# Optimization experiments

Hardware: AMD Instinct MI355X
Metric: run time of the kernel (lower is better)

Reference implementation:

```python
import jax, jax.numpy as jnp
import numpy as np

B, T, C, H = 8, 1024, 768, 12
HD = C // H  # 64

def setup_inputs() -> dict:
    key = jax.random.key(0)
    ks = jax.random.split(key, 5)
    s = 0.02
    return {
        "x": jax.random.normal(ks[0], (B, T, C), dtype=jnp.float32),
        "w_attn": jax.random.normal(ks[1], (C, 3 * C), dtype=jnp.float32) * s,
        "b_attn": jnp.zeros((3 * C,), dtype=jnp.float32),
        "w_proj": jax.random.normal(ks[2], (C, C), dtype=jnp.float32) * s,
        "b_proj": jnp.zeros((C,), dtype=jnp.float32),
    }

def reference(x, w_attn, b_attn, w_proj, b_proj):
    Bx, Tx, Cx = x.shape
    qkv = x @ w_attn + b_attn                      # [B,T,3C]
    q, k, v = jnp.split(qkv, 3, axis=-1)
    # [B,H,T,hd]
    q = q.reshape(Bx, Tx, H, HD).transpose(0, 2, 1, 3)
    k = k.reshape(Bx, Tx, H, HD).transpose(0, 2, 1, 3)
    v = v.reshape(Bx, Tx, H, HD).transpose(0, 2, 1, 3)
    scale = 1.0 / jnp.sqrt(jnp.asarray(HD, dtype=x.dtype))
    scores = jnp.einsum('bhqd,bhkd->bhqk', q, k) * scale  # [B,H,T,T]
    causal = jnp.tril(jnp.ones((Tx, Tx), dtype=bool))
    scores = jnp.where(causal, scores, jnp.asarray(-jnp.inf, dtype=x.dtype))
    weights = jax.nn.softmax(scores, axis=-1)
    y = jnp.einsum('bhqk,bhkd->bhqd', weights, v)  # [B,H,T,hd]
    y = y.transpose(0, 2, 1, 3).reshape(Bx, Tx, Cx)
    return y @ w_proj + b_proj
```

## Files before the change

kernel.cpp:

```cpp
#include <hip/hip_runtime.h>
#include <cstdint>
#include <cstddef>

#define B_  8
#define T_  1024
#define C_  768
#define H_  12
#define HD_ 64
#define K3_ 2304

typedef unsigned short u16;
typedef __attribute__((ext_vector_type(8))) short bf16x8;
typedef __attribute__((ext_vector_type(4))) float f32x4;

#define MFMA __builtin_amdgcn_mfma_f32_16x16x32_bf16

__device__ __forceinline__ u16 f2bf(float f) {
    unsigned u = __builtin_bit_cast(unsigned, f);
    u += 0x7fffu + ((u >> 16) & 1u);
    return (u16)(u >> 16);
}

__device__ __forceinline__ unsigned pk2bf(float a, float b) {
    unsigned ua = __builtin_bit_cast(unsigned, a) + 0x8000u;
    unsigned ub = __builtin_bit_cast(unsigned, b) + 0x8000u;
    return (ua >> 16) | (ub & 0xffff0000u);
}

#define GLL16(gp, lp) __builtin_amdgcn_global_load_lds( \
    (__attribute__((address_space(1))) unsigned int*)(gp), \
    (__attribute__((address_space(3))) unsigned int*)(lp), 16, 0, 0)

__global__ void cvt_f32_bf16(const float* __restrict__ in, u16* __restrict__ out, int n4) {
    int i = blockIdx.x * blockDim.x + threadIdx.x;
    if (i < n4) {
        float4 v = ((const float4*)in)[i];
        ushort4 o;
        o.x = f2bf(v.x); o.y = f2bf(v.y); o.z = f2bf(v.z); o.w = f2bf(v.w);
        ((ushort4*)out)[i] = o;
    }
}

__global__ void tcvt(const float* __restrict__ in, u16* __restrict__ out, int R, int Cc) {
    __shared__ float tile[32][33];
    int bc = blockIdx.x * 32, br = blockIdx.y * 32;
    int tx = threadIdx.x, ty = threadIdx.y;
    #pragma unroll
    for (int kk = 0; kk < 32; kk += 8)
        tile[ty + kk][tx] = in[(size_t)(br + ty + kk) * Cc + bc + tx];
    __syncthreads();
    #pragma unroll
    for (int kk = 0; kk < 32; kk += 8)
        out[(size_t)(bc + ty + kk) * R + br + tx] = f2bf(tile[tx][ty + kk]);
}

__launch_bounds__(256)
__global__ void gemm_qkv(const u16* __restrict__ A, const u16* __restrict__ Bt,
                         const float* __restrict__ bias,
                         u16* __restrict__ q, u16* __restrict__ k, u16* __restrict__ v) {
    const int K = C_;
    __shared__ __align__(16) u16 SM[16896];
    u16 (*As)[32] = (u16(*)[32])SM;
    u16 (*Bs)[32] = (u16(*)[32])(SM + 4096);
    u16 (*Cs)[132] = (u16(*)[132])SM;
    int tid = threadIdx.x;
    int m0 = blockIdx.y * 128, n0 = blockIdx.x * 128;
    int lane = tid & 63, wv = tid >> 6;
    int wm = (wv >> 1) * 64, wn = (wv & 1) * 64;
    int r16 = lane & 15, quad = lane >> 4;

    f32x4 acc[4][4] = {};
    int row = tid >> 2, colb = (tid & 3) * 8;
    const u16* Ag0 = A  + (size_t)(m0 + row) * K + colb;
    const u16* Ag1 = A  + (size_t)(m0 + 64 + row) * K + colb;
    const u16* Bg0 = Bt + (size_t)(n0 + row) * K + colb;
    const u16* Bg1 = Bt + (size_t)(n0 + 64 + row) * K + colb;
    u16* Al0 = &As[row][colb];
    u16* Al1 = &As[64 + row][colb];
    u16* Bl0 = &Bs[row][colb];
    u16* Bl1 = &Bs[64 + row][colb];

    for (int kt = 0; kt < K; kt += 32) {
        GLL16(Ag0 + kt, Al0);
        GLL16(Ag1 + kt, Al1);
        GLL16(Bg0 + kt, Bl0);
        GLL16(Bg1 + kt, Bl1);
        __syncthreads();
        bf16x8 af[4], bfr[4];
        #pragma unroll
        for (int i = 0; i < 4; i++) af[i]  = *(const bf16x8*)&As[wm + i * 16 + r16][quad * 8];
        #pragma unroll
        for (int j = 0; j < 4; j++) bfr[j] = *(const bf16x8*)&Bs[wn + j * 16 + r16][quad * 8];
        #pragma unroll
        for (int i = 0; i < 4; i++)
            #pragma unroll
            for (int j = 0; j < 4; j++)
                acc[i][j] = MFMA(af[i], bfr[j], acc[i][j], 0, 0, 0);
        __syncthreads();
    }

    int sec = n0 / C_;
    int cc0 = n0 - sec * C_;
    int b = m0 >> 10, t0 = m0 & 1023;

    if (sec == 2) {
        #pragma unroll
        for (int i = 0; i < 4; i++) {
            #pragma unroll
            for (int j = 0; j < 4; j++) {
                int cc = cc0 + wn + j * 16 + r16;
                float bv = bias[2 * C_ + cc];
                int h = cc >> 6, hd = cc & 63;
                int t = t0 + wm + i * 16 + quad * 4;
                ushort4 ov;
                ov.x = f2bf(acc[i][j][0] + bv); ov.y = f2bf(acc[i][j][1] + bv);
                ov.z = f2bf(acc[i][j][2] + bv); ov.w = f2bf(acc[i][j][3] + bv);
                *(ushort4*)(v + (((size_t)b * H_ + h) * HD_ + hd) * T_ + t) = ov;
            }
        }
    } else {
        float scale = (sec == 0) ? 0.125f : 1.0f;
        u16* dst = (sec == 0) ? q : k;
        #pragma unroll
        for (int i = 0; i < 4; i++)
            #pragma unroll
            for (int j = 0; j < 4; j++) {
                int col = wn + j * 16 + r16;
                float bv = bias[sec * C_ + cc0 + col];
                #pragma unroll
                for (int r = 0; r < 4; r++)
                    Cs[wm + i * 16 + quad * 4 + r][col] = f2bf((acc[i][j][r] + bv) * scale);
            }
        __syncthreads();
        int h0 = cc0 >> 6;
        int rsel = tid >> 4;
        int hs = (tid >> 3) & 1;
        int c8 = (tid & 7) * 8;
        #pragma unroll
        for (int p = 0; p < 8; p++) {
            int rl = p * 16 + rsel;
            uint4 val = *(const uint4*)&Cs[rl][hs * 64 + c8];
            *(uint4*)(dst + (((size_t)b * H_ + h0 + hs) * T_ + t0 + rl) * HD_ + c8) = val;
        }
    }
}

__launch_bounds__(256)
__global__ void gemm_proj(const u16* __restrict__ A, const u16* __restrict__ Bt,
                          const float* __restrict__ bias, float* __restrict__ out) {
    const int K = C_, N = C_;
    __shared__ __align__(16) u16 As[128][32];
    __shared__ __align__(16) u16 Bs[128][32];
    int tid = threadIdx.x;
    int m0 = blockIdx.y * 128, n0 = blockIdx.x * 128;
    int lane = tid & 63, wv = tid >> 6;
    int wm = (wv >> 1) * 64, wn = (wv & 1) * 64;
    int r16 = lane & 15, quad = lane >> 4;

    f32x4 acc[4][4] = {};
    int row = tid >> 2, colb = (tid & 3) * 8;
    const u16* Ag0 = A  + (size_t)(m0 + row) * K + colb;
    const u16* Ag1 = A  + (size_t)(m0 + 64 + row) * K + colb;
    const u16* Bg0 = Bt + (size_t)(n0 + row) * K + colb;
    const u16* Bg1 = Bt + (size_t)(n0 + 64 + row) * K + colb;
    u16* Al0 = &As[row][colb];
    u16* Al1 = &As[64 + row][colb];
    u16* Bl0 = &Bs[row][colb];
    u16* Bl1 = &Bs[64 + row][colb];

    for (int kt = 0; kt < K; kt += 32) {
        GLL16(Ag0 + kt, Al0);
        GLL16(Ag1 + kt, Al1);
        GLL16(Bg0 + kt, Bl0);
        GLL16(Bg1 + kt, Bl1);
        __syncthreads();
        bf16x8 af[4], bfr[4];
        #pragma unroll
        for (int i = 0; i < 4; i++) af[i]  = *(const bf16x8*)&As[wm + i * 16 + r16][quad * 8];
        #pragma unroll
        for (int j = 0; j < 4; j++) bfr[j] = *(const bf16x8*)&Bs[wn + j * 16 + r16][quad * 8];
        #pragma unroll
        for (int i = 0; i < 4; i++)
            #pragma unroll
            for (int j = 0; j < 4; j++)
                acc[i][j] = MFMA(af[i], bfr[j], acc[i][j], 0, 0, 0);
        __syncthreads();
    }

    #pragma unroll
    for (int i = 0; i < 4; i++) {
        #pragma unroll
        for (int j = 0; j < 4; j++) {
            int gn = n0 + wn + j * 16 + r16;
            float bv = bias[gn];
            #pragma unroll
            for (int r = 0; r < 4; r++) {
                int gm = m0 + wm + i * 16 + quad * 4 + r;
                out[(size_t)gm * N + gn] = acc[i][j][r] + bv;
            }
        }
    }
}

__launch_bounds__(256, 2)
__global__ void attn(const u16* __restrict__ q, const u16* __restrict__ k,
                     const u16* __restrict__ v, u16* __restrict__ y) {
    __shared__ __align__(16) u16 Kb[2][64][64];
    __shared__ __align__(16) u16 Vb[2][64][64];
    __shared__ __align__(16) u16 P[4][2][16][72];
    int tid = threadIdx.x, lane = tid & 63, w = tid >> 6;
    int r16 = lane & 15, quad = lane >> 4;
    int id = blockIdx.x;
    int bh = id % 96;
    int bi = id / 96;
    int b = bh / H_, h = bh - b * H_;
    int x = bi * 4 + w;
    int t_lo = x, t_hi = 63 - x;
    int qb_lo = t_lo * 16, qb_hi = t_hi * 16;
    const u16* qh = q + (size_t)bh * T_ * HD_;
    const u16* kh = k + (size_t)bh * T_ * HD_;
    const u16* vh = v + (size_t)bh * HD_ * T_;

    bf16x8 ql0 = *(const bf16x8*)(qh + (size_t)(qb_lo + r16) * HD_ + quad * 8);
    bf16x8 ql1 = *(const bf16x8*)(qh + (size_t)(qb_lo + r16) * HD_ + 32 + quad * 8);
    bf16x8 qh0 = *(const bf16x8*)(qh + (size_t)(qb_hi + r16) * HD_ + quad * 8);
    bf16x8 qh1 = *(const bf16x8*)(qh + (size_t)(qb_hi + r16) * HD_ + 32 + quad * 8);

    f32x4 oL[4] = {}, oH[4] = {};
    float lL = 0.f, lH = 0.f;
    int qyL = qb_lo + r16, qyH = qb_hi + r16;
    int ilo_last = bi;
    int n64 = __builtin_amdgcn_readfirstlane(16 - bi);

    int srow = lane >> 3;
    int scb  = (lane & 7) ^ srow;
    const u16* kst = kh + (size_t)(w * 16 + srow) * HD_ + scb * 8;
    const u16* vst = vh + (size_t)(w * 16 + srow) * T_ + scb * 8;
    int swz = (r16 & 7);

    {
        #pragma unroll
        for (int s2 = 0; s2 < 2; s2++) {
            GLL16(kst + (size_t)(s2 * 8) * HD_, &Kb[0][w * 16 + s2 * 8][0] + lane * 8);
            GLL16(vst + (size_t)(s2 * 8) * T_,  &Vb[0][w * 16 + s2 * 8][0] + lane * 8);
        }
    }
    __syncthreads();

    for (int it = 0; it < n64; ++it) {
        int kv0 = it * 64;
        int buf = it & 1;
        bool lo_on = (it <= ilo_last);
        if (it + 1 < n64) {
            int kvn = kv0 + 64;
            #pragma unroll
            for (int s2 = 0; s2 < 2; s2++) {
                GLL16(kst + (size_t)(kvn + s2 * 8) * HD_, &Kb[buf ^ 1][w * 16 + s2 * 8][0] + lane * 8);
                GLL16(vst + (size_t)(s2 * 8) * T_ + kvn,  &Vb[buf ^ 1][w * 16 + s2 * 8][0] + lane * 8);
            }
        }
        bf16x8 kf[4][2];
        #pragma unroll
        for (int n = 0; n < 4; n++)
            #pragma unroll
            for (int c = 0; c < 2; c++)
                kf[n][c] = *(const bf16x8*)&Kb[buf][n * 16 + r16][((c * 4 + quad) ^ swz) * 8];
        f32x4 sH[4] = {};
        #pragma unroll
        for (int n = 0; n < 4; n++) {
            sH[n] = MFMA(kf[n][0], qh0, sH[n], 0, 0, 0);
            sH[n] = MFMA(kf[n][1], qh1, sH[n], 0, 0, 0);
        }
        if (it == n64 - 1) {
            #pragma unroll
            for (int n = 0; n < 4; n++)
                #pragma unroll
                for (int r = 0; r < 4; r++)
                    if (kv0 + n * 16 + quad * 4 + r > qyH) sH[n][r] = -1e30f;
        }
        #pragma unroll
        for (int n = 0; n < 4; n++) {
            float p0 = __expf(sH[n][0]);
            float p1 = __expf(sH[n][1]);
            float p2 = __expf(sH[n][2]);
            float p3 = __expf(sH[n][3]);
            lH += (p0 + p1) + (p2 + p3);
            uint2 pd; pd.x = pk2bf(p0, p1); pd.y = pk2bf(p2, p3);
            *(uint2*)&P[w][1][r16][n * 16 + quad * 4] = pd;
        }
        if (lo_on) {
            f32x4 sL[4] = {};
            #pragma unroll
            for (int n = 0; n < 4; n++) {
                sL[n] = MFMA(kf[n][0], ql0, sL[n], 0, 0, 0);
                sL[n] = MFMA(kf[n][1], ql1, sL[n], 0, 0, 0);
            }
            if (it == ilo_last) {
                #pragma unroll
                for (int n = 0; n < 4; n++)
                    #pragma unroll
                    for (int r = 0; r < 4; r++)
                        if (kv0 + n * 16 + quad * 4 + r > qyL) sL[n][r] = -1e30f;
            }
            #pragma unroll
            for (int n = 0; n < 4; n++) {
                float p0 = __expf(sL[n][0]);
                float p1 = __expf(sL[n][1]);
                float p2 = __expf(sL[n][2]);
                float p3 = __expf(sL[n][3]);
                lL += (p0 + p1) + (p2 + p3);
                uint2 pd; pd.x = pk2bf(p0, p1); pd.y = pk2bf(p2, p3);
                *(uint2*)&P[w][0][r16][n * 16 + quad * 4] = pd;
            }
        }
        bf16x8 vf[4][2];
        #pragma unroll
        for (int j = 0; j < 4; j++)
            #pragma unroll
            for (int c = 0; c < 2; c++)
                vf[j][c] = *(const bf16x8*)&Vb[buf][j * 16 + r16][((c * 4 + quad) ^ swz) * 8];
        #pragma unroll
        for (int c = 0; c < 2; c++) {
            bf16x8 pfH = *(const bf16x8*)&P[w][1][r16][c * 32 + quad * 8];
            #pragma unroll
            for (int j = 0; j < 4; j++)
                oH[j] = MFMA(vf[j][c], pfH, oH[j], 0, 0, 0);
        }
        if (lo_on) {
            #pragma unroll
            for (int c = 0; c < 2; c++) {
                bf16x8 pfL = *(const bf16x8*)&P[w][0][r16][c * 32 + quad * 8];
                #pragma unroll
                for (int j = 0; j < 4; j++)
                    oL[j] = MFMA(vf[j][c], pfL, oL[j], 0, 0, 0);
            }
        }
        __syncthreads();
    }

    lH += __shfl_xor(lH, 16, 64);
    lH += __shfl_xor(lH, 32, 64);
    lL += __shfl_xor(lL, 16, 64);
    lL += __shfl_xor(lL, 32, 64);
    float invH = 1.f / lH, invL = 1.f / lL;
    int tqH = qb_hi + r16, tqL = qb_lo + r16;
    #pragma unroll
    for (int j = 0; j < 4; j++) {
        ushort4 ovH, ovL;
        ovH.x = f2bf(oH[j][0] * invH); ovH.y = f2bf(oH[j][1] * invH);
        ovH.z = f2bf(oH[j][2] * invH); ovH.w = f2bf(oH[j][3] * invH);
        ovL.x = f2bf(oL[j][0] * invL); ovL.y = f2bf(oL[j][1] * invL);
        ovL.z = f2bf(oL[j][2] * invL); ovL.w = f2bf(oL[j][3] * invL);
        *(ushort4*)(y + ((size_t)b * T_ + tqH) * C_ + h * 64 + j * 16 + quad * 4) = ovH;
        *(ushort4*)(y + ((size_t)b * T_ + tqL) * C_ + h * 64 + j * 16 + quad * 4) = ovL;
    }
}

extern "C" void kernel_launch(void* const* d_in, const int* in_sizes, int n_in,
                              void* d_out, int out_size, void* d_ws, size_t ws_size,
                              hipStream_t stream) {
    const float* x      = (const float*)d_in[0];
    const float* w_attn = (const float*)d_in[1];
    const float* b_attn = (const float*)d_in[2];
    const float* w_proj = (const float*)d_in[3];
    const float* b_proj = (const float*)d_in[4];
    float* out = (float*)d_out;

    char* ws = (char*)d_ws;
    size_t off = 0;
    auto alloc = [&](size_t bytes) {
        void* p = ws + off;
        off += (bytes + 255) & ~(size_t)255;
        return p;
    };
    const size_t M = (size_t)B_ * T_;
    u16* x_bf = (u16*)alloc(M * C_ * 2);
    u16* wat  = (u16*)alloc((size_t)K3_ * C_ * 2);
    u16* wpt  = (u16*)alloc((size_t)C_ * C_ * 2);
    u16* qb   = (u16*)alloc((size_t)B_ * H_ * T_ * HD_ * 2);
    u16* kb   = (u16*)alloc((size_t)B_ * H_ * T_ * HD_ * 2);
    u16* vb   = (u16*)alloc((size_t)B_ * H_ * T_ * HD_ * 2);
    u16* yb   = (u16*)alloc(M * C_ * 2);

    cvt_f32_bf16<<<(int)(M * C_ / 4 / 256), 256, 0, stream>>>(x, x_bf, (int)(M * C_ / 4));
    tcvt<<<dim3(K3_ / 32, C_ / 32), dim3(32, 8), 0, stream>>>(w_attn, wat, C_, K3_);
    tcvt<<<dim3(C_ / 32, C_ / 32), dim3(32, 8), 0, stream>>>(w_proj, wpt, C_, C_);
    gemm_qkv<<<dim3(K3_ / 128, (int)(M / 128)), 256, 0, stream>>>(x_bf, wat, b_attn, qb, kb, vb);
    attn<<<dim3(8 * 96), 256, 0, stream>>>(qb, kb, vb, yb);
    gemm_proj<<<dim3(C_ / 128, (int)(M / 128)), 256, 0, stream>>>(yb, wpt, b_proj, out);
}
```

Baseline: 197.3 us.

## Fuse conversion kernels, widen GEMM K-tile with swizzled LDS, remap blocks per XCD

Merges the three input/weight conversion launches into a single prep kernel that dispatches by block index. Both GEMMs now stage a 64-wide K tile per iteration, so there are half as many barriers, and use an XOR swizzle on LDS rows to avoid bank conflicts on the fragment reads. Blocks are also remapped onto a 1D grid so that consecutive blocks on each XCD share M tiles, which should improve L2 reuse. The trade-offs are more LDS per block and a hardcoded grid mapping that relies on 8 XCDs.

Result: faster. 175.6 us (-11.0%).

```diff
diff --git a/kernel.cpp b/kernel.cpp
--- a/kernel.cpp
+++ b/kernel.cpp
@@ -31,27 +31,37 @@
     (__attribute__((address_space(1))) unsigned int*)(gp), \
     (__attribute__((address_space(3))) unsigned int*)(lp), 16, 0, 0)
 
-__global__ void cvt_f32_bf16(const float* __restrict__ in, u16* __restrict__ out, int n4) {
-    int i = blockIdx.x * blockDim.x + threadIdx.x;
-    if (i < n4) {
-        float4 v = ((const float4*)in)[i];
-        ushort4 o;
-        o.x = f2bf(v.x); o.y = f2bf(v.y); o.z = f2bf(v.z); o.w = f2bf(v.w);
-        ((ushort4*)out)[i] = o;
-    }
-}
-
-__global__ void tcvt(const float* __restrict__ in, u16* __restrict__ out, int R, int Cc) {
-    __shared__ float tile[32][33];
-    int bc = blockIdx.x * 32, br = blockIdx.y * 32;
-    int tx = threadIdx.x, ty = threadIdx.y;
+__device__ __forceinline__ void tcvt_tile(const float* __restrict__ in, u16* __restrict__ out,
+                                          int R, int Cc, int bx, int by, int tid, float* tile ) {
+    int bc = bx * 32, br = by * 32;
+    int tx = tid & 31, ty = tid >> 5;
     #pragma unroll
     for (int kk = 0; kk < 32; kk += 8)
-        tile[ty + kk][tx] = in[(size_t)(br + ty + kk) * Cc + bc + tx];
+        tile[(ty + kk) * 33 + tx] = in[(size_t)(br + ty + kk) * Cc + bc + tx];
     __syncthreads();
     #pragma unroll
     for (int kk = 0; kk < 32; kk += 8)
-        out[(size_t)(bc + ty + kk) * R + br + tx] = f2bf(tile[tx][ty + kk]);
+        out[(size_t)(bc + ty + kk) * R + br + tx] = f2bf(tile[tx * 33 + ty + kk]);
+}
+
+__global__ void prep(const float* __restrict__ x, u16* __restrict__ xb,
+                     const float* __restrict__ wa, u16* __restrict__ wat,
+                     const float* __restrict__ wp, u16* __restrict__ wpt) {
+    __shared__ float tile[32 * 33];
+    int bid = blockIdx.x, tid = threadIdx.x;
+    if (bid < 6144) {
+        int i = bid * 256 + tid;
+        float4 v = ((const float4*)x)[i];
+        ushort4 o;
+        o.x = f2bf(v.x); o.y = f2bf(v.y); o.z = f2bf(v.z); o.w = f2bf(v.w);
+        ((ushort4*)xb)[i] = o;
+    } else if (bid < 6144 + 1728) {
+        int b = bid - 6144;
+        tcvt_tile(wa, wat, C_, K3_, b % 72, b / 72, tid, tile);
+    } else {
+        int b = bid - 7872;
+        tcvt_tile(wp, wpt, C_, C_, b % 24, b / 24, tid, tile);
+    }
 }
 
 __launch_bounds__(256)
@@ -60,42 +70,47 @@
                          u16* __restrict__ q, u16* __restrict__ k, u16* __restrict__ v) {
     const int K = C_;
     __shared__ __align__(16) u16 SM[16896];
-    u16 (*As)[32] = (u16(*)[32])SM;
-    u16 (*Bs)[32] = (u16(*)[32])(SM + 4096);
+    u16 (*As)[64] = (u16(*)[64])SM;
+    u16 (*Bs)[64] = (u16(*)[64])(SM + 8192);
     u16 (*Cs)[132] = (u16(*)[132])SM;
     int tid = threadIdx.x;
-    int m0 = blockIdx.y * 128, n0 = blockIdx.x * 128;
+    int id = blockIdx.x;
+    int xcd = id & 7, jj = id >> 3;
+    int m0 = (xcd * 8 + (jj & 7)) * 128;
+    int n0 = (jj >> 3) * 128;
     int lane = tid & 63, wv = tid >> 6;
     int wm = (wv >> 1) * 64, wn = (wv & 1) * 64;
     int r16 = lane & 15, quad = lane >> 4;
 
     f32x4 acc[4][4] = {};
-    int row = tid >> 2, colb = (tid & 3) * 8;
-    const u16* Ag0 = A  + (size_t)(m0 + row) * K + colb;
-    const u16* Ag1 = A  + (size_t)(m0 + 64 + row) * K + colb;
-    const u16* Bg0 = Bt + (size_t)(n0 + row) * K + colb;
-    const u16* Bg1 = Bt + (size_t)(n0 + 64 + row) * K + colb;
-    u16* Al0 = &As[row][colb];
-    u16* Al1 = &As[64 + row][colb];
-    u16* Bl0 = &Bs[row][colb];
-    u16* Bl1 = &Bs[64 + row][colb];
-
-    for (int kt = 0; kt < K; kt += 32) {
-        GLL16(Ag0 + kt, Al0);
-        GLL16(Ag1 + kt, Al1);
-        GLL16(Bg0 + kt, Bl0);
-        GLL16(Bg1 + kt, Bl1);
-        __syncthreads();
-        bf16x8 af[4], bfr[4];
-        #pragma unroll
-        for (int i = 0; i < 4; i++) af[i]  = *(const bf16x8*)&As[wm + i * 16 + r16][quad * 8];
-        #pragma unroll
-        for (int j = 0; j < 4; j++) bfr[j] = *(const bf16x8*)&Bs[wn + j * 16 + r16][quad * 8];
-        #pragma unroll
-        for (int i = 0; i < 4; i++)
-            #pragma unroll
-            for (int j = 0; j < 4; j++)
-                acc[i][j] = MFMA(af[i], bfr[j], acc[i][j], 0, 0, 0);
+    int srow = tid >> 3;
+    int gblk = (tid & 7) ^ (srow & 7);
+    const u16* Ag = A  + (size_t)(m0 + srow) * K + gblk * 8;
+    const u16* Bg = Bt + (size_t)(n0 + srow) * K + gblk * 8;
+    u16* Al = SM + tid * 8;
+    u16* Bl = SM + 8192 + tid * 8;
+    int sw = r16 & 7;
+
+    for (int kt = 0; kt < K; kt += 64) {
+        #pragma unroll
+        for (int s = 0; s < 4; s++) {
+            GLL16(Ag + (size_t)(s * 32) * K + kt, Al + s * 2048);
+            GLL16(Bg + (size_t)(s * 32) * K + kt, Bl + s * 2048);
+        }
+        __syncthreads();
+        #pragma unroll
+        for (int kk = 0; kk < 2; kk++) {
+            bf16x8 af[4], bfr[4];
+            #pragma unroll
+            for (int i = 0; i < 4; i++) af[i]  = *(const bf16x8*)&As[wm + i * 16 + r16][((kk * 4 + quad) ^ sw) * 8];
+            #pragma unroll
+            for (int j = 0; j < 4; j++) bfr[j] = *(const bf16x8*)&Bs[wn + j * 16 + r16][((kk * 4 + quad) ^ sw) * 8];
+            #pragma unroll
+            for (int i = 0; i < 4; i++)
+                #pragma unroll
+                for (int j = 0; j < 4; j++)
+                    acc[i][j] = MFMA(af[i], bfr[j], acc[i][j], 0, 0, 0);
+        }
         __syncthreads();
     }
 
@@ -149,41 +164,47 @@
 __global__ void gemm_proj(const u16* __restrict__ A, const u16* __restrict__ Bt,
                           const float* __restrict__ bias, float* __restrict__ out) {
     const int K = C_, N = C_;
-    __shared__ __align__(16) u16 As[128][32];
-    __shared__ __align__(16) u16 Bs[128][32];
+    __shared__ __align__(16) u16 SM[16384];
+    u16 (*As)[64] = (u16(*)[64])SM;
+    u16 (*Bs)[64] = (u16(*)[64])(SM + 8192);
     int tid = threadIdx.x;
-    int m0 = blockIdx.y * 128, n0 = blockIdx.x * 128;
+    int id = blockIdx.x;
+    int xcd = id & 7, jj = id >> 3;
+    int m0 = (xcd * 8 + (jj & 7)) * 128;
+    int n0 = (jj >> 3) * 128;
     int lane = tid & 63, wv = tid >> 6;
     int wm = (wv >> 1) * 64, wn = (wv & 1) * 64;
     int r16 = lane & 15, quad = lane >> 4;
 
     f32x4 acc[4][4] = {};
-    int row = tid >> 2, colb = (tid & 3) * 8;
-    const u16* Ag0 = A  + (size_t)(m0 + row) * K + colb;
-    const u16* Ag1 = A  + (size_t)(m0 + 64 + row) * K + colb;
-    const u16* Bg0 = Bt + (size_t)(n0 + row) * K + colb;
-    const u16* Bg1 = Bt + (size_t)(n0 + 64 + row) * K + colb;
-    u16* Al0 = &As[row][colb];
-    u16* Al1 = &As[64 + row][colb];
-    u16* Bl0 = &Bs[row][colb];
-    u16* Bl1 = &Bs[64 + row][colb];
-
-    for (int kt = 0; kt < K; kt += 32) {
-        GLL16(Ag0 + kt, Al0);
-        GLL16(Ag1 + kt, Al1);
-        GLL16(Bg0 + kt, Bl0);
-        GLL16(Bg1 + kt, Bl1);
-        __syncthreads();
-        bf16x8 af[4], bfr[4];
-        #pragma unroll
-        for (int i = 0; i < 4; i++) af[i]  = *(const bf16x8*)&As[wm + i * 16 + r16][quad * 8];
-        #pragma unroll
-        for (int j = 0; j < 4; j++) bfr[j] = *(const bf16x8*)&Bs[wn + j * 16 + r16][quad * 8];
-        #pragma unroll
-        for (int i = 0; i < 4; i++)
-            #pragma unroll
-            for (int j = 0; j < 4; j++)
-                acc[i][j] = MFMA(af[i], bfr[j], acc[i][j], 0, 0, 0);
+    int srow = tid >> 3;
+    int gblk = (tid & 7) ^ (srow & 7);
+    const u16* Ag = A  + (size_t)(m0 + srow) * K + gblk * 8;
+    const u16* Bg = Bt + (size_t)(n0 + srow) * K + gblk * 8;
+    u16* Al = SM + tid * 8;
+    u16* Bl = SM + 8192 + tid * 8;
+    int sw = r16 & 7;
+
+    for (int kt = 0; kt < K; kt += 64) {
+        #pragma unroll
+        for (int s = 0; s < 4; s++) {
+            GLL16(Ag + (size_t)(s * 32) * K + kt, Al + s * 2048);
+            GLL16(Bg + (size_t)(s * 32) * K + kt, Bl + s * 2048);
+        }
+        __syncthreads();
+        #pragma unroll
+        for (int kk = 0; kk < 2; kk++) {
+            bf16x8 af[4], bfr[4];
+            #pragma unroll
+            for (int i = 0; i < 4; i++) af[i]  = *(const bf16x8*)&As[wm + i * 16 + r16][((kk * 4 + quad) ^ sw) * 8];
+            #pragma unroll
+            for (int j = 0; j < 4; j++) bfr[j] = *(const bf16x8*)&Bs[wn + j * 16 + r16][((kk * 4 + quad) ^ sw) * 8];
+            #pragma unroll
+            for (int i = 0; i < 4; i++)
+                #pragma unroll
+                for (int j = 0; j < 4; j++)
+                    acc[i][j] = MFMA(af[i], bfr[j], acc[i][j], 0, 0, 0);
+        }
         __syncthreads();
     }
 
@@ -382,10 +403,8 @@
     u16* vb   = (u16*)alloc((size_t)B_ * H_ * T_ * HD_ * 2);
     u16* yb   = (u16*)alloc(M * C_ * 2);
 
-    cvt_f32_bf16<<<(int)(M * C_ / 4 / 256), 256, 0, stream>>>(x, x_bf, (int)(M * C_ / 4));
-    tcvt<<<dim3(K3_ / 32, C_ / 32), dim3(32, 8), 0, stream>>>(w_attn, wat, C_, K3_);
-    tcvt<<<dim3(C_ / 32, C_ / 32), dim3(32, 8), 0, stream>>>(w_proj, wpt, C_, C_);
-    gemm_qkv<<<dim3(K3_ / 128, (int)(M / 128)), 256, 0, stream>>>(x_bf, wat, b_attn, qb, kb, vb);
-    attn<<<dim3(8 * 96), 256, 0, stream>>>(qb, kb, vb, yb);
-    gemm_proj<<<dim3(C_ / 128, (int)(M / 128)), 256, 0, stream>>>(yb, wpt, b_proj, out);
-}
+    prep<<<6144 + 1728 + 576, 256, 0, stream>>>(x, x_bf, w_attn, wat, w_proj, wpt);
+    gemm_qkv<<<8 * 144, 256, 0, stream>>>(x_bf, wat, b_attn, qb, kb, vb);
+    attn<<<8 * 96, 256, 0, stream>>>(qb, kb, vb, yb);
+    gemm_proj<<<8 * 48, 256, 0, stream>>>(yb, wpt, b_proj, out);
+}
```
